# Kernel optimization log

Measured on AMD Instinct MI355X. Metric: run time of the kernel, lower is better.

The kernel has to match this reference:

```python
import jax, jax.numpy as jnp
import numpy as np

B, L1, L2 = 4, 2048, 2048
INP1_DIM = INP2_DIM = 1024
QK_DIM = V_DIM = 1024
HEAD_N = 16
QK_HEAD = QK_DIM // HEAD_N  # 64
V_HEAD = V_DIM // HEAD_N    # 64
SCALE = 1.0 / (QK_HEAD ** 0.5)


def _linear_params(key, out_dim, in_dim):
    # torch nn.Linear default init: U(-1/sqrt(in), 1/sqrt(in)) for W and b
    kw, kb = jax.random.split(key)
    bound = 1.0 / np.sqrt(in_dim)
    W = jax.random.uniform(kw, (out_dim, in_dim), jnp.float32, -bound, bound)
    b = jax.random.uniform(kb, (out_dim,), jnp.float32, -bound, bound)
    return W, b


def setup_inputs() -> dict:
    key = jax.random.key(0)
    k1, k2, kq, kk, kv = jax.random.split(key, 5)
    inp1 = jax.random.normal(k1, (B, L1, INP1_DIM), jnp.float32)
    inp2 = jax.random.normal(k2, (B, L2, INP2_DIM), jnp.float32)
    Wq, bq = _linear_params(kq, QK_DIM, INP1_DIM)
    Wk, bk = _linear_params(kk, QK_DIM, INP2_DIM)
    Wv, bv = _linear_params(kv, V_DIM, INP2_DIM)
    return {"inp1": inp1, "inp2": inp2, "Wq": Wq, "bq": bq,
            "Wk": Wk, "bk": bk, "Wv": Wv, "bv": bv,
            "rescale_with_score": 1}


def reference(inp1, inp2, Wq, bq, Wk, bk, Wv, bv, rescale_with_score):
    b, l1, _ = inp1.shape
    l2 = inp2.shape[1]
    # torch Linear: x @ W.T + b
    q = (jnp.einsum('bld,ed->ble', inp1, Wq) + bq).reshape(b, l1, HEAD_N, QK_HEAD)
    k = (jnp.einsum('bmd,ed->bme', inp2, Wk) + bk).reshape(b, l2, HEAD_N, QK_HEAD)
    v = (jnp.einsum('bmd,ed->bme', inp2, Wv) + bv).reshape(b, l2, HEAD_N, V_HEAD)
    # scores: [b, l1, l2, h], softmax over l2 (axis=2)
    s = jax.nn.softmax(jnp.einsum('blhd,bmhd->blmh', q, k) * SCALE, axis=2)
    res = jnp.einsum('blmh,bmhd->blhd', s, v)  # [b, l1, h, v_head]
    if rescale_with_score:
        # per-query, per-head sum of squared attention weights -> [b, l1, h, 1]
        denom = jnp.sqrt(jnp.sum(s * s, axis=2))[..., None]
        res = res / denom
    return res.reshape(b, l1, -1)
```

## Files before the change

kernel.cpp:

```cpp
#include <hip/hip_runtime.h>
#include <hip/hip_bf16.h>

#define HEADS   16
#define HD      64
#define DMODEL  1024
#define LQ      2048
#define LK      2048
#define BATCH   4
#define MROWS   8192

typedef __attribute__((ext_vector_type(8))) short short8;
typedef __attribute__((ext_vector_type(4))) float f32x4;
typedef __attribute__((ext_vector_type(16))) float f32x16;
typedef __attribute__((ext_vector_type(2))) unsigned int uint2v;
typedef __attribute__((ext_vector_type(2))) short bf16x2;

union V4u { unsigned u[4]; short8 s8; };

static __device__ __forceinline__ unsigned short f2bf(float f) {
  unsigned u = __builtin_bit_cast(unsigned, f);
  u = (u + 0x7FFFu + ((u >> 16) & 1u)) >> 16;
  return (unsigned short)u;
}

static __device__ __forceinline__ unsigned cvtpk(float lo, float hi) {
  unsigned w;
  asm("v_cvt_pk_bf16_f32 %0, %1, %2" : "=v"(w) : "v"(lo), "v"(hi));
  return w;
}

static __device__ __forceinline__ void permswap(unsigned &a, unsigned &b) {
  asm volatile("v_permlane32_swap_b32 %0, %1" : "+v"(a), "+v"(b));
}

static __device__ __forceinline__ void gload_lds16(const void* g, void* l) {
  __builtin_amdgcn_global_load_lds(
      (const __attribute__((address_space(1))) unsigned int*)g,
      (__attribute__((address_space(3))) unsigned int*)l, 16, 0, 0);
}

static __device__ __forceinline__ unsigned lds_addr(const void* p) {
  return (unsigned)(size_t)(const __attribute__((address_space(3))) void*)p;
}

static __device__ __forceinline__ void ds_read128o(unsigned addr, int imm, V4u &d) {
  asm volatile("ds_read_b128 %0, %1 offset:%c2" : "=v"(d.s8) : "v"(addr), "i"(imm));
}

static __device__ __forceinline__ void ds_read_tro(unsigned addr, int imm, uint2v &d) {
  asm volatile("ds_read_b64_tr_b16 %0, %1 offset:%c2" : "=v"(d) : "v"(addr), "i"(imm));
}

#if __has_builtin(__builtin_amdgcn_fdot2_f32_bf16)
#define HAVE_BF16_DOT2 1
static __device__ __forceinline__ float dot2_sq(unsigned w, float acc) {
  bf16x2 v = __builtin_bit_cast(bf16x2, w);
  return __builtin_amdgcn_fdot2_f32_bf16(v, v, acc, false);
}
static __device__ __forceinline__ float dot2_sum(unsigned w, float acc) {
  bf16x2 ones = __builtin_bit_cast(bf16x2, 0x3F803F80u);
  bf16x2 v = __builtin_bit_cast(bf16x2, w);
  return __builtin_amdgcn_fdot2_f32_bf16(v, ones, acc, false);
}
#else
#define HAVE_BF16_DOT2 0
#endif

__global__ void cvt_in_kernel(const float* __restrict__ s0, unsigned short* __restrict__ d0,
                              const float* __restrict__ s1, unsigned short* __restrict__ d1,
                              int n4) {
  int i = blockIdx.x * blockDim.x + threadIdx.x;
  if (i >= n4) return;
  const float* s = blockIdx.y ? s1 : s0;
  unsigned short* d = blockIdx.y ? d1 : d0;
  float4 v = ((const float4*)s)[i];
  ushort4 o;
  o.x = f2bf(v.x); o.y = f2bf(v.y); o.z = f2bf(v.z); o.w = f2bf(v.w);
  ((ushort4*)d)[i] = o;
}

__global__ void cvt_w_kernel(const float* __restrict__ s0, unsigned short* __restrict__ d0,
                             const float* __restrict__ s1, unsigned short* __restrict__ d1,
                             const float* __restrict__ s2, unsigned short* __restrict__ d2,
                             float scale0, int n4) {
  int i = blockIdx.x * blockDim.x + threadIdx.x;
  if (i >= n4) return;
  const float* s = blockIdx.y == 0 ? s0 : (blockIdx.y == 1 ? s1 : s2);
  unsigned short* d = blockIdx.y == 0 ? d0 : (blockIdx.y == 1 ? d1 : d2);
  float sc = blockIdx.y == 0 ? scale0 : 1.0f;
  float4 v = ((const float4*)s)[i];
  ushort4 o;
  o.x = f2bf(v.x * sc); o.y = f2bf(v.y * sc); o.z = f2bf(v.z * sc); o.w = f2bf(v.w * sc);
  ((ushort4*)d)[i] = o;
}

__global__ __launch_bounds__(256, 4) void gemm3_kernel(
    const unsigned short* __restrict__ X1,
    const unsigned short* __restrict__ X2,
    const unsigned short* __restrict__ Wqb,
    const unsigned short* __restrict__ Wkb,
    const unsigned short* __restrict__ Wvb,
    const float* __restrict__ bq,
    const float* __restrict__ bk,
    const float* __restrict__ bv,
    unsigned short* __restrict__ Qb,
    unsigned short* __restrict__ Kb,
    unsigned short* __restrict__ Vb,
    float cexp) {
  __shared__ __attribute__((aligned(16))) unsigned short As[128 * 32];
  __shared__ __attribute__((aligned(16))) unsigned short Bs[128 * 32];
  const int sel = blockIdx.z;
  const unsigned short* A = (sel == 0) ? X1 : X2;
  const unsigned short* W = (sel == 0) ? Wqb : (sel == 1) ? Wkb : Wvb;
  const float* bias = (sel == 0) ? bq : (sel == 1) ? bk : bv;
  unsigned short* C = (sel == 0) ? Qb : (sel == 1) ? Kb : Vb;
  const float bscale = (sel == 0) ? cexp : 1.0f;

  const int tid = threadIdx.x;
  const int l = tid & 63, w = tid >> 6;
  const int c = l & 15, g = l >> 4;
  const int wm = w >> 1, wn = w & 1;
  const int m0 = blockIdx.x * 128, n0 = blockIdx.y * 128;

  f32x4 acc[4][4];
#pragma unroll
  for (int i = 0; i < 4; ++i)
#pragma unroll
    for (int j = 0; j < 4; ++j) acc[i][j] = (f32x4){0.f, 0.f, 0.f, 0.f};

  for (int k0 = 0; k0 < 1024; k0 += 32) {
#pragma unroll
    for (int is = 0; is < 2; ++is) {
      int lin = is * 256 + tid;
      int r = lin >> 2, s = lin & 3;
      int gofs = (s ^ (r & 3)) * 8;
      gload_lds16(A + (size_t)(m0 + r) * 1024 + k0 + gofs,
                  &As[(is * 256 + (tid & ~63)) * 8]);
      gload_lds16(W + (size_t)(n0 + r) * 1024 + k0 + gofs,
                  &Bs[(is * 256 + (tid & ~63)) * 8]);
    }
    __syncthreads();
    short8 af[4], bfr[4];
#pragma unroll
    for (int mt = 0; mt < 4; ++mt) {
      int row = wm * 64 + mt * 16 + c;
      af[mt] = *(const short8*)((const char*)As + row * 64 + ((g ^ (row & 3)) << 4));
    }
#pragma unroll
    for (int nt = 0; nt < 4; ++nt) {
      int row = wn * 64 + nt * 16 + c;
      bfr[nt] = *(const short8*)((const char*)Bs + row * 64 + ((g ^ (row & 3)) << 4));
    }
    __builtin_amdgcn_s_setprio(1);
#pragma unroll
    for (int mt = 0; mt < 4; ++mt)
#pragma unroll
      for (int nt = 0; nt < 4; ++nt)
        acc[mt][nt] = __builtin_amdgcn_mfma_f32_16x16x32_bf16(af[mt], bfr[nt], acc[mt][nt], 0, 0, 0);
    __builtin_amdgcn_s_setprio(0);
    __syncthreads();
  }
  float bv4[4];
#pragma unroll
  for (int nt = 0; nt < 4; ++nt) bv4[nt] = bias[n0 + wn * 64 + nt * 16 + c] * bscale;
#pragma unroll
  for (int mt = 0; mt < 4; ++mt)
#pragma unroll
    for (int nt = 0; nt < 4; ++nt)
#pragma unroll
      for (int r = 0; r < 4; ++r) {
        int m = m0 + wm * 64 + mt * 16 + g * 4 + r;
        int n = n0 + wn * 64 + nt * 16 + c;
        C[(size_t)m * 1024 + n] = f2bf(acc[mt][nt][r] + bv4[nt]);
      }
}

__global__ __launch_bounds__(512) void attn_kernel(
    const unsigned short* __restrict__ Q,
    const unsigned short* __restrict__ K,
    const unsigned short* __restrict__ V,
    float* __restrict__ out,
    const int* __restrict__ rescale_flag) {
  __shared__ __attribute__((aligned(16))) unsigned short Kbuf[2][64 * 64];
  __shared__ __attribute__((aligned(16))) unsigned short Vbuf[2][64 * 64];
  __shared__ float ivLds[8][32];

  const int tid = threadIdx.x;
  const int lane = tid & 63, w = tid >> 6;
  const int l31 = lane & 31, hi = lane >> 5;

  const int gid = blockIdx.x;
  const int xcd = gid & 7;
  const int o = gid >> 3;
  const int bh = xcd * 8 + (o >> 3);
  const int qb = o & 7;
  const int bb = bh >> 4, h = bh & 15;
  const size_t qrowb = (size_t)bb * LQ + qb * 256 + w * 32;

  const int rs = *rescale_flag;

  short8 qf[4];
#pragma unroll
  for (int ks = 0; ks < 4; ++ks)
    qf[ks] = *(const short8*)(Q + (qrowb + l31) * 1024 + h * 64 + ks * 16 + hi * 8);

  const size_t kvbase = (size_t)bb * LK * 1024 + (size_t)h * 64;
  const int k_kv = w * 8 + (lane >> 3);
  const int k_sl = (lane & 7) ^ (lane >> 3);
  const unsigned short* ksrc0 = K + kvbase + (size_t)k_kv * 1024 + k_sl * 8;
  const int v_kv = (w & 3) * 16 + ((lane >> 4) & 1) * 8 + ((lane >> 5) & 1) * 4 + ((lane >> 1) & 3);
  const int v_d  = (w >> 2) * 32 + ((lane >> 3) & 1) * 16 + (lane & 1) * 8;
  const unsigned short* vsrc0 = V + kvbase + (size_t)v_kv * 1024 + v_d;

  unsigned koff[4];
#pragma unroll
  for (int ks = 0; ks < 4; ++ks)
    koff[ks] = (unsigned)(l31 * 128 + ((((ks << 1) | hi) ^ (l31 & 7)) << 4));
  const unsigned kbase0 = lds_addr(&Kbuf[0][0]);
  const unsigned vbase0 = lds_addr(&Vbuf[0][0]);

  f32x16 po[2];
  po[0] = {}; po[1] = {};
  float za0 = 0.f, za1 = 0.f, s20 = 0.f, s21 = 0.f;

  gload_lds16(ksrc0, &Kbuf[0][w * 512]);
  gload_lds16(vsrc0, &Vbuf[0][w * 512]);
  __syncthreads();

  int cur = 0;
  for (int t = 0; t < LK / 64; ++t) {
    if (t < LK / 64 - 1) {
      gload_lds16(ksrc0 + (size_t)(t + 1) * 65536, &Kbuf[cur ^ 1][w * 512]);
      gload_lds16(vsrc0 + (size_t)(t + 1) * 65536, &Vbuf[cur ^ 1][w * 512]);
    }
    unsigned kaddr[4];
#pragma unroll
    for (int ks = 0; ks < 4; ++ks) kaddr[ks] = kbase0 + (unsigned)(cur * 8192) + koff[ks];
    const unsigned vtr = vbase0 + (unsigned)(cur * 8192) + (unsigned)(lane * 8);

#pragma unroll
    for (int s = 0; s < 2; ++s) {
      V4u kfr[4];
#pragma unroll
      for (int ks = 0; ks < 4; ++ks) ds_read128o(kaddr[ks], s * 4096, kfr[ks]);
      uint2v ta0, ta1, ta2, ta3, tb0, tb1, tb2, tb3;
      ds_read_tro(vtr, (2 * s) * 1024, ta0);
      ds_read_tro(vtr, (2 * s) * 1024 + 512, ta1);
      ds_read_tro(vtr, (2 * s) * 1024 + 4096, ta2);
      ds_read_tro(vtr, (2 * s) * 1024 + 4608, ta3);
      ds_read_tro(vtr, (2 * s + 1) * 1024, tb0);
      ds_read_tro(vtr, (2 * s + 1) * 1024 + 512, tb1);
      ds_read_tro(vtr, (2 * s + 1) * 1024 + 4096, tb2);
      ds_read_tro(vtr, (2 * s + 1) * 1024 + 4608, tb3);
      asm volatile("s_waitcnt lgkmcnt(8)" ::: "memory");
      __builtin_amdgcn_sched_barrier(0);
      f32x16 ps = {};
      __builtin_amdgcn_s_setprio(1);
      ps = __builtin_amdgcn_mfma_f32_32x32x16_bf16(kfr[0].s8, qf[0], ps, 0, 0, 0);
      ps = __builtin_amdgcn_mfma_f32_32x32x16_bf16(kfr[1].s8, qf[1], ps, 0, 0, 0);
      ps = __builtin_amdgcn_mfma_f32_32x32x16_bf16(kfr[2].s8, qf[2], ps, 0, 0, 0);
      ps = __builtin_amdgcn_mfma_f32_32x32x16_bf16(kfr[3].s8, qf[3], ps, 0, 0, 0);
      __builtin_amdgcn_s_setprio(0);
      float p[16];
#pragma unroll
      for (int r = 0; r < 16; ++r) p[r] = __builtin_amdgcn_exp2f(ps[r]);
      unsigned wlo[4], whi[4];
#pragma unroll
      for (int b = 0; b < 4; ++b) {
        wlo[b] = cvtpk(p[4 * b + 0], p[4 * b + 1]);
        whi[b] = cvtpk(p[4 * b + 2], p[4 * b + 3]);
      }
#if HAVE_BF16_DOT2
      if (rs) {
#pragma unroll
        for (int b = 0; b < 4; ++b) {
          s20 = dot2_sq(wlo[b], s20);
          s21 = dot2_sq(whi[b], s21);
        }
      } else {
#pragma unroll
        for (int b = 0; b < 4; ++b) {
          za0 = dot2_sum(wlo[b], za0);
          za1 = dot2_sum(whi[b], za1);
        }
      }
#else
      if (rs) {
#pragma unroll
        for (int r = 0; r < 8; ++r) {
          s20 = fmaf(p[2 * r], p[2 * r], s20);
          s21 = fmaf(p[2 * r + 1], p[2 * r + 1], s21);
        }
      } else {
#pragma unroll
        for (int r = 0; r < 8; ++r) {
          za0 += p[2 * r];
          za1 += p[2 * r + 1];
        }
      }
#endif
      {
        unsigned a0 = wlo[0], b0 = wlo[1], a1 = whi[0], b1 = whi[1];
        permswap(a0, b0);
        permswap(a1, b1);
        V4u pau; pau.u[0] = a0; pau.u[1] = a1; pau.u[2] = b0; pau.u[3] = b1;
        asm volatile("s_waitcnt lgkmcnt(4)" ::: "memory");
        __builtin_amdgcn_sched_barrier(0);
        V4u v0u, v1u;
        v0u.u[0] = ta0[0]; v0u.u[1] = ta0[1]; v0u.u[2] = ta1[0]; v0u.u[3] = ta1[1];
        v1u.u[0] = ta2[0]; v1u.u[1] = ta2[1]; v1u.u[2] = ta3[0]; v1u.u[3] = ta3[1];
        __builtin_amdgcn_s_setprio(1);
        po[0] = __builtin_amdgcn_mfma_f32_32x32x16_bf16(pau.s8, v0u.s8, po[0], 0, 0, 0);
        po[1] = __builtin_amdgcn_mfma_f32_32x32x16_bf16(pau.s8, v1u.s8, po[1], 0, 0, 0);
        __builtin_amdgcn_s_setprio(0);
      }
      {
        unsigned a0 = wlo[2], b0 = wlo[3], a1 = whi[2], b1 = whi[3];
        permswap(a0, b0);
        permswap(a1, b1);
        V4u pau; pau.u[0] = a0; pau.u[1] = a1; pau.u[2] = b0; pau.u[3] = b1;
        asm volatile("s_waitcnt lgkmcnt(0)" ::: "memory");
        __builtin_amdgcn_sched_barrier(0);
        V4u v0u, v1u;
        v0u.u[0] = tb0[0]; v0u.u[1] = tb0[1]; v0u.u[2] = tb1[0]; v0u.u[3] = tb1[1];
        v1u.u[0] = tb2[0]; v1u.u[1] = tb2[1]; v1u.u[2] = tb3[0]; v1u.u[3] = tb3[1];
        __builtin_amdgcn_s_setprio(1);
        po[0] = __builtin_amdgcn_mfma_f32_32x32x16_bf16(pau.s8, v0u.s8, po[0], 0, 0, 0);
        po[1] = __builtin_amdgcn_mfma_f32_32x32x16_bf16(pau.s8, v1u.s8, po[1], 0, 0, 0);
        __builtin_amdgcn_s_setprio(0);
      }
    }
    __syncthreads();
    cur ^= 1;
  }

  float zacc = za0 + za1;
  float s2acc = s20 + s21;
  float z2 = zacc + __shfl_xor(zacc, 32, 64);
  float s22 = s2acc + __shfl_xor(s2acc, 32, 64);
  float iv = rs ? (1.0f / sqrtf(s22)) : (1.0f / z2);
  ivLds[w][l31] = iv;

#pragma unroll
  for (int dt = 0; dt < 2; ++dt)
#pragma unroll
    for (int r = 0; r < 16; ++r) {
      const int ql = (r & 3) + 8 * (r >> 2) + 4 * hi;
      out[(qrowb + ql) * 1024 + h * 64 + dt * 32 + l31] = po[dt][r] * ivLds[w][ql];
    }
}

extern "C" void kernel_launch(void* const* d_in, const int* in_sizes, int n_in,
                              void* d_out, int out_size, void* d_ws, size_t ws_size,
                              hipStream_t stream) {
  const float* inp1 = (const float*)d_in[0];
  const float* inp2 = (const float*)d_in[1];
  const float* Wq = (const float*)d_in[2];
  const float* bq = (const float*)d_in[3];
  const float* Wk = (const float*)d_in[4];
  const float* bk = (const float*)d_in[5];
  const float* Wv = (const float*)d_in[6];
  const float* bv = (const float*)d_in[7];
  const int* rs = (const int*)d_in[8];
  float* out = (float*)d_out;

  const float CEXP = 0.18033688011112042f;

  unsigned short* X1  = (unsigned short*)d_ws;
  unsigned short* X2  = X1 + (size_t)MROWS * 1024;
  unsigned short* Wqb = X2 + (size_t)MROWS * 1024;
  unsigned short* Wkb = Wqb + (size_t)1024 * 1024;
  unsigned short* Wvb = Wkb + (size_t)1024 * 1024;
  unsigned short* Qb  = Wvb + (size_t)1024 * 1024;
  unsigned short* Kb  = Qb + (size_t)MROWS * 1024;
  unsigned short* Vb  = Kb + (size_t)MROWS * 1024;

  cvt_in_kernel<<<dim3(MROWS * 1024 / 1024, 2), 256, 0, stream>>>(inp1, X1, inp2, X2, MROWS * 1024 / 4);
  cvt_w_kernel<<<dim3(1024, 3), 256, 0, stream>>>(Wq, Wqb, Wk, Wkb, Wv, Wvb, CEXP, 1024 * 1024 / 4);

  gemm3_kernel<<<dim3(64, 8, 3), 256, 0, stream>>>(X1, X2, Wqb, Wkb, Wvb,
                                                   bq, bk, bv, Qb, Kb, Vb, CEXP);

  attn_kernel<<<dim3(512), 512, 0, stream>>>(Qb, Kb, Vb, out, rs);
}
```

Baseline: 159.5 us.

## Process 64 query rows per wave with 2-wave blocks in attention kernel

```diff
diff --git a/kernel.cpp b/kernel.cpp
--- a/kernel.cpp
+++ b/kernel.cpp
@@ -175,7 +175,7 @@
       }
 }
 
-__global__ __launch_bounds__(512) void attn_kernel(
+__global__ __launch_bounds__(128, 4) void attn_kernel(
     const unsigned short* __restrict__ Q,
     const unsigned short* __restrict__ K,
     const unsigned short* __restrict__ V,
@@ -183,7 +183,7 @@
     const int* __restrict__ rescale_flag) {
   __shared__ __attribute__((aligned(16))) unsigned short Kbuf[2][64 * 64];
   __shared__ __attribute__((aligned(16))) unsigned short Vbuf[2][64 * 64];
-  __shared__ float ivLds[8][32];
+  __shared__ float ivLds[2][64];
 
   const int tid = threadIdx.x;
   const int lane = tid & 63, w = tid >> 6;
@@ -192,25 +192,26 @@
   const int gid = blockIdx.x;
   const int xcd = gid & 7;
   const int o = gid >> 3;
-  const int bh = xcd * 8 + (o >> 3);
-  const int qb = o & 7;
+  const int bh = xcd * 8 + (o >> 4);
+  const int qb = o & 15;
   const int bb = bh >> 4, h = bh & 15;
-  const size_t qrowb = (size_t)bb * LQ + qb * 256 + w * 32;
+  const size_t qrowb = (size_t)bb * LQ + qb * 128 + w * 64;
 
   const int rs = *rescale_flag;
 
-  short8 qf[4];
-#pragma unroll
-  for (int ks = 0; ks < 4; ++ks)
-    qf[ks] = *(const short8*)(Q + (qrowb + l31) * 1024 + h * 64 + ks * 16 + hi * 8);
+  short8 qf0[4], qf1[4];
+#pragma unroll
+  for (int ks = 0; ks < 4; ++ks) {
+    qf0[ks] = *(const short8*)(Q + (qrowb + l31) * 1024 + h * 64 + ks * 16 + hi * 8);
+    qf1[ks] = *(const short8*)(Q + (qrowb + 32 + l31) * 1024 + h * 64 + ks * 16 + hi * 8);
+  }
 
   const size_t kvbase = (size_t)bb * LK * 1024 + (size_t)h * 64;
-  const int k_kv = w * 8 + (lane >> 3);
-  const int k_sl = (lane & 7) ^ (lane >> 3);
-  const unsigned short* ksrc0 = K + kvbase + (size_t)k_kv * 1024 + k_sl * 8;
-  const int v_kv = (w & 3) * 16 + ((lane >> 4) & 1) * 8 + ((lane >> 5) & 1) * 4 + ((lane >> 1) & 3);
-  const int v_d  = (w >> 2) * 32 + ((lane >> 3) & 1) * 16 + (lane & 1) * 8;
-  const unsigned short* vsrc0 = V + kvbase + (size_t)v_kv * 1024 + v_d;
+  const unsigned short* ksrc0 =
+      K + kvbase + (size_t)(w * 8 + (lane >> 3)) * 1024 + ((lane & 7) ^ (lane >> 3)) * 8;
+  const int v_kv0 = w * 16 + ((lane >> 4) & 1) * 8 + ((lane >> 5) & 1) * 4 + ((lane >> 1) & 3);
+  const int v_d0  = ((lane >> 3) & 1) * 16 + (lane & 1) * 8;
+  const unsigned short* vsrc0 = V + kvbase + (size_t)v_kv0 * 1024 + v_d0;
 
   unsigned koff[4];
 #pragma unroll
@@ -219,19 +220,29 @@
   const unsigned kbase0 = lds_addr(&Kbuf[0][0]);
   const unsigned vbase0 = lds_addr(&Vbuf[0][0]);
 
-  f32x16 po[2];
-  po[0] = {}; po[1] = {};
-  float za0 = 0.f, za1 = 0.f, s20 = 0.f, s21 = 0.f;
-
-  gload_lds16(ksrc0, &Kbuf[0][w * 512]);
-  gload_lds16(vsrc0, &Vbuf[0][w * 512]);
+#define STAGE_KV(buf, adv)                                                          \
+  {                                                                                 \
+    _Pragma("unroll")                                                               \
+    for (int r = 0; r < 4; ++r) {                                                   \
+      gload_lds16(ksrc0 + (adv) + (size_t)r * 16384,                                \
+                  &Kbuf[buf][(r * 128 + w * 64) * 8]);                              \
+      gload_lds16(vsrc0 + (adv) + (size_t)(r & 1) * 32768 + (r >> 1) * 32,          \
+                  &Vbuf[buf][(r * 128 + w * 64) * 8]);                              \
+    }                                                                               \
+  }
+
+  f32x16 po00, po01, po10, po11;
+  po00 = (f32x16){}; po01 = (f32x16){}; po10 = (f32x16){}; po11 = (f32x16){};
+  float za0g0 = 0.f, za1g0 = 0.f, s20g0 = 0.f, s21g0 = 0.f;
+  float za0g1 = 0.f, za1g1 = 0.f, s20g1 = 0.f, s21g1 = 0.f;
+
+  STAGE_KV(0, 0);
   __syncthreads();
 
   int cur = 0;
   for (int t = 0; t < LK / 64; ++t) {
     if (t < LK / 64 - 1) {
-      gload_lds16(ksrc0 + (size_t)(t + 1) * 65536, &Kbuf[cur ^ 1][w * 512]);
-      gload_lds16(vsrc0 + (size_t)(t + 1) * 65536, &Vbuf[cur ^ 1][w * 512]);
+      STAGE_KV(cur ^ 1, (size_t)(t + 1) * 65536);
     }
     unsigned kaddr[4];
 #pragma unroll
@@ -254,79 +265,115 @@
       ds_read_tro(vtr, (2 * s + 1) * 1024 + 4608, tb3);
       asm volatile("s_waitcnt lgkmcnt(8)" ::: "memory");
       __builtin_amdgcn_sched_barrier(0);
-      f32x16 ps = {};
+      f32x16 ps0 = {}, ps1 = {};
       __builtin_amdgcn_s_setprio(1);
-      ps = __builtin_amdgcn_mfma_f32_32x32x16_bf16(kfr[0].s8, qf[0], ps, 0, 0, 0);
-      ps = __builtin_amdgcn_mfma_f32_32x32x16_bf16(kfr[1].s8, qf[1], ps, 0, 0, 0);
-      ps = __builtin_amdgcn_mfma_f32_32x32x16_bf16(kfr[2].s8, qf[2], ps, 0, 0, 0);
-      ps = __builtin_amdgcn_mfma_f32_32x32x16_bf16(kfr[3].s8, qf[3], ps, 0, 0, 0);
+      ps0 = __builtin_amdgcn_mfma_f32_32x32x16_bf16(kfr[0].s8, qf0[0], ps0, 0, 0, 0);
+      ps1 = __builtin_amdgcn_mfma_f32_32x32x16_bf16(kfr[0].s8, qf1[0], ps1, 0, 0, 0);
+      ps0 = __builtin_amdgcn_mfma_f32_32x32x16_bf16(kfr[1].s8, qf0[1], ps0, 0, 0, 0);
+      ps1 = __builtin_amdgcn_mfma_f32_32x32x16_bf16(kfr[1].s8, qf1[1], ps1, 0, 0, 0);
+      ps0 = __builtin_amdgcn_mfma_f32_32x32x16_bf16(kfr[2].s8, qf0[2], ps0, 0, 0, 0);
+      ps1 = __builtin_amdgcn_mfma_f32_32x32x16_bf16(kfr[2].s8, qf1[2], ps1, 0, 0, 0);
+      ps0 = __builtin_amdgcn_mfma_f32_32x32x16_bf16(kfr[3].s8, qf0[3], ps0, 0, 0, 0);
+      ps1 = __builtin_amdgcn_mfma_f32_32x32x16_bf16(kfr[3].s8, qf1[3], ps1, 0, 0, 0);
       __builtin_amdgcn_s_setprio(0);
-      float p[16];
-#pragma unroll
-      for (int r = 0; r < 16; ++r) p[r] = __builtin_amdgcn_exp2f(ps[r]);
-      unsigned wlo[4], whi[4];
-#pragma unroll
-      for (int b = 0; b < 4; ++b) {
-        wlo[b] = cvtpk(p[4 * b + 0], p[4 * b + 1]);
-        whi[b] = cvtpk(p[4 * b + 2], p[4 * b + 3]);
-      }
+      unsigned wlo0[4], whi0[4], wlo1[4], whi1[4];
+      {
+        float p[16];
+#pragma unroll
+        for (int r = 0; r < 16; ++r) p[r] = __builtin_amdgcn_exp2f(ps0[r]);
+#pragma unroll
+        for (int b = 0; b < 4; ++b) {
+          wlo0[b] = cvtpk(p[4 * b + 0], p[4 * b + 1]);
+          whi0[b] = cvtpk(p[4 * b + 2], p[4 * b + 3]);
+        }
 #if HAVE_BF16_DOT2
-      if (rs) {
-#pragma unroll
-        for (int b = 0; b < 4; ++b) {
-          s20 = dot2_sq(wlo[b], s20);
-          s21 = dot2_sq(whi[b], s21);
-        }
-      } else {
-#pragma unroll
-        for (int b = 0; b < 4; ++b) {
-          za0 = dot2_sum(wlo[b], za0);
-          za1 = dot2_sum(whi[b], za1);
-        }
-      }
+        if (rs) {
+#pragma unroll
+          for (int b = 0; b < 4; ++b) { s20g0 = dot2_sq(wlo0[b], s20g0); s21g0 = dot2_sq(whi0[b], s21g0); }
+        } else {
+#pragma unroll
+          for (int b = 0; b < 4; ++b) { za0g0 = dot2_sum(wlo0[b], za0g0); za1g0 = dot2_sum(whi0[b], za1g0); }
+        }
 #else
-      if (rs) {
-#pragma unroll
-        for (int r = 0; r < 8; ++r) {
-          s20 = fmaf(p[2 * r], p[2 * r], s20);
-          s21 = fmaf(p[2 * r + 1], p[2 * r + 1], s21);
-        }
-      } else {
-#pragma unroll
-        for (int r = 0; r < 8; ++r) {
-          za0 += p[2 * r];
-          za1 += p[2 * r + 1];
-        }
-      }
+        if (rs) {
+#pragma unroll
+          for (int r = 0; r < 8; ++r) { s20g0 = fmaf(p[2 * r], p[2 * r], s20g0); s21g0 = fmaf(p[2 * r + 1], p[2 * r + 1], s21g0); }
+        } else {
+#pragma unroll
+          for (int r = 0; r < 8; ++r) { za0g0 += p[2 * r]; za1g0 += p[2 * r + 1]; }
+        }
 #endif
-      {
-        unsigned a0 = wlo[0], b0 = wlo[1], a1 = whi[0], b1 = whi[1];
-        permswap(a0, b0);
-        permswap(a1, b1);
+      }
+      V4u v0u, v1u;
+      {
+        unsigned a0 = wlo0[0], b0 = wlo0[1], a1 = whi0[0], b1 = whi0[1];
+        permswap(a0, b0); permswap(a1, b1);
         V4u pau; pau.u[0] = a0; pau.u[1] = a1; pau.u[2] = b0; pau.u[3] = b1;
         asm volatile("s_waitcnt lgkmcnt(4)" ::: "memory");
         __builtin_amdgcn_sched_barrier(0);
-        V4u v0u, v1u;
         v0u.u[0] = ta0[0]; v0u.u[1] = ta0[1]; v0u.u[2] = ta1[0]; v0u.u[3] = ta1[1];
         v1u.u[0] = ta2[0]; v1u.u[1] = ta2[1]; v1u.u[2] = ta3[0]; v1u.u[3] = ta3[1];
         __builtin_amdgcn_s_setprio(1);
-        po[0] = __builtin_amdgcn_mfma_f32_32x32x16_bf16(pau.s8, v0u.s8, po[0], 0, 0, 0);
-        po[1] = __builtin_amdgcn_mfma_f32_32x32x16_bf16(pau.s8, v1u.s8, po[1], 0, 0, 0);
+        po00 = __builtin_amdgcn_mfma_f32_32x32x16_bf16(pau.s8, v0u.s8, po00, 0, 0, 0);
+        po01 = __builtin_amdgcn_mfma_f32_32x32x16_bf16(pau.s8, v1u.s8, po01, 0, 0, 0);
         __builtin_amdgcn_s_setprio(0);
       }
       {
-        unsigned a0 = wlo[2], b0 = wlo[3], a1 = whi[2], b1 = whi[3];
-        permswap(a0, b0);
-        permswap(a1, b1);
+        float p[16];
+#pragma unroll
+        for (int r = 0; r < 16; ++r) p[r] = __builtin_amdgcn_exp2f(ps1[r]);
+#pragma unroll
+        for (int b = 0; b < 4; ++b) {
+          wlo1[b] = cvtpk(p[4 * b + 0], p[4 * b + 1]);
+          whi1[b] = cvtpk(p[4 * b + 2], p[4 * b + 3]);
+        }
+#if HAVE_BF16_DOT2
+        if (rs) {
+#pragma unroll
+          for (int b = 0; b < 4; ++b) { s20g1 = dot2_sq(wlo1[b], s20g1); s21g1 = dot2_sq(whi1[b], s21g1); }
+        } else {
+#pragma unroll
+          for (int b = 0; b < 4; ++b) { za0g1 = dot2_sum(wlo1[b], za0g1); za1g1 = dot2_sum(whi1[b], za1g1); }
+        }
+#else
+        if (rs) {
+#pragma unroll
+          for (int r = 0; r < 8; ++r) { s20g1 = fmaf(p[2 * r], p[2 * r], s20g1); s21g1 = fmaf(p[2 * r + 1], p[2 * r + 1], s21g1); }
+        } else {
+#pragma unroll
+          for (int r = 0; r < 8; ++r) { za0g1 += p[2 * r]; za1g1 += p[2 * r + 1]; }
+        }
+#endif
+      }
+      {
+        unsigned a0 = wlo1[0], b0 = wlo1[1], a1 = whi1[0], b1 = whi1[1];
+        permswap(a0, b0); permswap(a1, b1);
+        V4u pau; pau.u[0] = a0; pau.u[1] = a1; pau.u[2] = b0; pau.u[3] = b1;
+        __builtin_amdgcn_s_setprio(1);
+        po10 = __builtin_amdgcn_mfma_f32_32x32x16_bf16(pau.s8, v0u.s8, po10, 0, 0, 0);
+        po11 = __builtin_amdgcn_mfma_f32_32x32x16_bf16(pau.s8, v1u.s8, po11, 0, 0, 0);
+        __builtin_amdgcn_s_setprio(0);
+      }
+      {
+        unsigned a0 = wlo0[2], b0 = wlo0[3], a1 = whi0[2], b1 = whi0[3];
+        permswap(a0, b0); permswap(a1, b1);
         V4u pau; pau.u[0] = a0; pau.u[1] = a1; pau.u[2] = b0; pau.u[3] = b1;
         asm volatile("s_waitcnt lgkmcnt(0)" ::: "memory");
         __builtin_amdgcn_sched_barrier(0);
-        V4u v0u, v1u;
         v0u.u[0] = tb0[0]; v0u.u[1] = tb0[1]; v0u.u[2] = tb1[0]; v0u.u[3] = tb1[1];
         v1u.u[0] = tb2[0]; v1u.u[1] = tb2[1]; v1u.u[2] = tb3[0]; v1u.u[3] = tb3[1];
         __builtin_amdgcn_s_setprio(1);
-        po[0] = __builtin_amdgcn_mfma_f32_32x32x16_bf16(pau.s8, v0u.s8, po[0], 0, 0, 0);
-        po[1] = __builtin_amdgcn_mfma_f32_32x32x16_bf16(pau.s8, v1u.s8, po[1], 0, 0, 0);
+        po00 = __builtin_amdgcn_mfma_f32_32x32x16_bf16(pau.s8, v0u.s8, po00, 0, 0, 0);
+        po01 = __builtin_amdgcn_mfma_f32_32x32x16_bf16(pau.s8, v1u.s8, po01, 0, 0, 0);
+        __builtin_amdgcn_s_setprio(0);
+      }
+      {
+        unsigned a0 = wlo1[2], b0 = wlo1[3], a1 = whi1[2], b1 = whi1[3];
+        permswap(a0, b0); permswap(a1, b1);
+        V4u pau; pau.u[0] = a0; pau.u[1] = a1; pau.u[2] = b0; pau.u[3] = b1;
+        __builtin_amdgcn_s_setprio(1);
+        po10 = __builtin_amdgcn_mfma_f32_32x32x16_bf16(pau.s8, v0u.s8, po10, 0, 0, 0);
+        po11 = __builtin_amdgcn_mfma_f32_32x32x16_bf16(pau.s8, v1u.s8, po11, 0, 0, 0);
         __builtin_amdgcn_s_setprio(0);
       }
     }
@@ -334,20 +381,27 @@
     cur ^= 1;
   }
 
-  float zacc = za0 + za1;
-  float s2acc = s20 + s21;
-  float z2 = zacc + __shfl_xor(zacc, 32, 64);
-  float s22 = s2acc + __shfl_xor(s2acc, 32, 64);
-  float iv = rs ? (1.0f / sqrtf(s22)) : (1.0f / z2);
-  ivLds[w][l31] = iv;
-
-#pragma unroll
-  for (int dt = 0; dt < 2; ++dt)
-#pragma unroll
-    for (int r = 0; r < 16; ++r) {
-      const int ql = (r & 3) + 8 * (r >> 2) + 4 * hi;
-      out[(qrowb + ql) * 1024 + h * 64 + dt * 32 + l31] = po[dt][r] * ivLds[w][ql];
-    }
+  {
+    float zacc = za0g0 + za1g0, s2acc = s20g0 + s21g0;
+    float z2 = zacc + __shfl_xor(zacc, 32, 64);
+    float s22 = s2acc + __shfl_xor(s2acc, 32, 64);
+    ivLds[w][l31] = rs ? (1.0f / sqrtf(s22)) : (1.0f / z2);
+  }
+  {
+    float zacc = za0g1 + za1g1, s2acc = s20g1 + s21g1;
+    float z2 = zacc + __shfl_xor(zacc, 32, 64);
+    float s22 = s2acc + __shfl_xor(s2acc, 32, 64);
+    ivLds[w][32 + l31] = rs ? (1.0f / sqrtf(s22)) : (1.0f / z2);
+  }
+
+#pragma unroll
+  for (int r = 0; r < 16; ++r) {
+    const int cr = (r & 3) + 8 * (r >> 2) + 4 * hi;
+    out[(qrowb + cr) * 1024 + h * 64 + l31] = po00[r] * ivLds[w][cr];
+    out[(qrowb + cr) * 1024 + h * 64 + 32 + l31] = po01[r] * ivLds[w][cr];
+    out[(qrowb + 32 + cr) * 1024 + h * 64 + l31] = po10[r] * ivLds[w][32 + cr];
+    out[(qrowb + 32 + cr) * 1024 + h * 64 + 32 + l31] = po11[r] * ivLds[w][32 + cr];
+  }
 }
 
 extern "C" void kernel_launch(void* const* d_in, const int* in_sizes, int n_in,
@@ -381,5 +435,5 @@
   gemm3_kernel<<<dim3(64, 8, 3), 256, 0, stream>>>(X1, X2, Wqb, Wkb, Wvb,
                                                    bq, bk, bv, Qb, Kb, Vb, CEXP);
 
-  attn_kernel<<<dim3(512), 512, 0, stream>>>(Qb, Kb, Vb, out, rs);
-}
+  attn_kernel<<<dim3(1024), 128, 0, stream>>>(Qb, Kb, Vb, out, rs);
+}
```

After: 171.0 us. +7.2%, slower.
